# Kernel optimization log

Hardware: AMD Instinct MI355X
Metric: run time of the kernel (lower is better)

## Reference

```python
import jax, jax.numpy as jnp
import numpy as np

N_NODES = 50000
N_EDGES = 800000
NFEAT, NHID, NOUT = 512, 256, 64


def setup_inputs() -> dict:
    key = jax.random.key(0)
    ks = jax.random.split(key, 8)
    x = jax.random.normal(ks[0], (N_NODES, NFEAT), dtype=jnp.float32)
    w1 = jax.random.normal(ks[1], (NFEAT, NHID), dtype=jnp.float32) * (1.0 / np.sqrt(NFEAT))
    b1 = jnp.zeros((NHID,), dtype=jnp.float32)
    w2 = jax.random.normal(ks[2], (NHID, NOUT), dtype=jnp.float32) * (1.0 / np.sqrt(NHID))
    b2 = jnp.zeros((NOUT,), dtype=jnp.float32)
    edge_w = jax.random.uniform(ks[3], (N_EDGES,), dtype=jnp.float32)
    row = jnp.sort(jax.random.randint(ks[4], (N_EDGES,), 0, N_NODES, dtype=jnp.int32))
    col = jax.random.randint(ks[5], (N_EDGES,), 0, N_NODES, dtype=jnp.int32)
    return {"x": x, "w1": w1, "b1": b1, "w2": w2, "b2": b2,
            "edge_w": edge_w, "row": row, "col": col}


def _spmm(edge_w, row, col, h, n_nodes):
    # sparse adj (COO) @ dense h : gather source rows, scale, scatter-add to dest
    msgs = h[col] * edge_w[:, None]          # [E, d]
    return jax.ops.segment_sum(msgs, row, num_segments=n_nodes)


def reference(x, w1, b1, w2, b2, edge_w, row, col):
    n = x.shape[0]
    # layer 1: support = x @ W1; out = adj @ support + b1; relu
    h = jnp.matmul(x, w1)                    # [N, nhid]
    h = _spmm(edge_w, row, col, h, n) + b1
    h = jax.nn.relu(h)
    # layer 2
    h = jnp.matmul(h, w2)                    # [N, nout]
    out = _spmm(edge_w, row, col, h, n) + b2
    return out
```

## Files before the change

kernel.cpp:

```cpp
#include <hip/hip_runtime.h>

#define N_NODES 50000
#define MP      50048
#define N_EDGES 800000
#define NFEAT   512
#define NHID    256
#define NOUT    64

typedef __bf16 bf16x8 __attribute__((ext_vector_type(8)));
typedef float  f32x4  __attribute__((ext_vector_type(4)));

#define GLOAD_LDS16(g, l) __builtin_amdgcn_global_load_lds(                    \
    (const __attribute__((address_space(1))) void*)(g),                        \
    (__attribute__((address_space(3))) void*)(l), 16, 0, 0)

__device__ __forceinline__ unsigned short f2bf(float f) {
    __bf16 b = (__bf16)f;
    return __builtin_bit_cast(unsigned short, b);
}

__global__ void build_rowptr(const int* __restrict__ row, int* __restrict__ rp) {
    int r = blockIdx.x * blockDim.x + threadIdx.x;
    if (r > N_NODES) return;
    int lo = 0, hi = N_EDGES;
    while (lo < hi) {
        int mid = (lo + hi) >> 1;
        if (row[mid] < r) lo = mid + 1; else hi = mid;
    }
    rp[r] = lo;
}

__global__ __launch_bounds__(256) void conv_x(const float* __restrict__ x,
                                              __bf16* __restrict__ xb) {
    size_t i = ((size_t)blockIdx.x * 256 + threadIdx.x) * 8;
    unsigned short u[8];
    if (i < (size_t)N_NODES * NFEAT) {
        float4 a = *(const float4*)(x + i);
        float4 b = *(const float4*)(x + i + 4);
        u[0] = f2bf(a.x); u[1] = f2bf(a.y); u[2] = f2bf(a.z); u[3] = f2bf(a.w);
        u[4] = f2bf(b.x); u[5] = f2bf(b.y); u[6] = f2bf(b.z); u[7] = f2bf(b.w);
    } else {
        #pragma unroll
        for (int j = 0; j < 8; j++) u[j] = 0;
    }
    uint4 o;
    o.x = (unsigned)u[0] | ((unsigned)u[1] << 16);
    o.y = (unsigned)u[2] | ((unsigned)u[3] << 16);
    o.z = (unsigned)u[4] | ((unsigned)u[5] << 16);
    o.w = (unsigned)u[6] | ((unsigned)u[7] << 16);
    *(uint4*)(xb + i) = o;
}

__global__ void conv_w1t(const float* __restrict__ w1, __bf16* __restrict__ w1t) {
    int o = blockIdx.x * blockDim.x + threadIdx.x;
    int n = o >> 9, k = o & 511;
    w1t[o] = (__bf16)w1[(size_t)k * NHID + n];
}

__global__ void conv_w2t(const float* __restrict__ w2, __bf16* __restrict__ w2t) {
    int o = blockIdx.x * blockDim.x + threadIdx.x;
    int n = o >> 8, k = o & 255;
    w2t[o] = (__bf16)w2[(size_t)k * NOUT + n];
}

__global__ void zero_h1pad(__bf16* __restrict__ h1) {
    int i = blockIdx.x * blockDim.x + threadIdx.x;
    h1[(size_t)N_NODES * NHID + i] = (__bf16)0.f;
}

__global__ __launch_bounds__(256) void gemm1_mfma(const __bf16* __restrict__ A,
                                                  const __bf16* __restrict__ Bt,
                                                  __bf16* __restrict__ C) {
    __shared__ __bf16 As[128 * 32];
    __shared__ __bf16 Bs[128 * 32];
    const int t = threadIdx.x;
    const int w = t >> 6, l = t & 63;
    const int wm = w >> 1, wn = w & 1;
    const int ml = l & 15, quad = l >> 4;
    const int row0 = blockIdx.x * 128;
    const int col0 = blockIdx.y * 128;

    f32x4 acc[4][4] = {};

    for (int k0 = 0; k0 < NFEAT; k0 += 32) {
        #pragma unroll
        for (int i = 0; i < 2; i++) {
            int q = (w * 2 + i) * 64 + l;
            int r = q >> 2, cc = (q & 3) * 8;
            GLOAD_LDS16(A  + (size_t)(row0 + r) * NFEAT + k0 + cc, As + (w * 2 + i) * 512);
            GLOAD_LDS16(Bt + (size_t)(col0 + r) * NFEAT + k0 + cc, Bs + (w * 2 + i) * 512);
        }
        __syncthreads();
        bf16x8 af[4], bfr[4];
        #pragma unroll
        for (int mi = 0; mi < 4; mi++)
            af[mi] = *(const bf16x8*)(As + (wm * 64 + mi * 16 + ml) * 32 + quad * 8);
        #pragma unroll
        for (int ni = 0; ni < 4; ni++)
            bfr[ni] = *(const bf16x8*)(Bs + (wn * 64 + ni * 16 + ml) * 32 + quad * 8);
        #pragma unroll
        for (int mi = 0; mi < 4; mi++)
            #pragma unroll
            for (int ni = 0; ni < 4; ni++)
                acc[mi][ni] = __builtin_amdgcn_mfma_f32_16x16x32_bf16(
                    af[mi], bfr[ni], acc[mi][ni], 0, 0, 0);
        __syncthreads();
    }

    #pragma unroll
    for (int mi = 0; mi < 4; mi++) {
        int gr = row0 + wm * 64 + mi * 16 + quad * 4;
        #pragma unroll
        for (int ni = 0; ni < 4; ni++) {
            int gc = col0 + wn * 64 + ni * 16 + ml;
            #pragma unroll
            for (int r2 = 0; r2 < 4; r2++)
                C[(size_t)(gr + r2) * NHID + gc] = (__bf16)acc[mi][ni][r2];
        }
    }
}

__global__ __launch_bounds__(256) void gemm2_mfma(const __bf16* __restrict__ A,
                                                  const __bf16* __restrict__ Bt,
                                                  float* __restrict__ C) {
    __shared__ __bf16 As[128 * 32];
    __shared__ __bf16 Bs[64 * 32];
    const int t = threadIdx.x;
    const int w = t >> 6, l = t & 63;
    const int ml = l & 15, quad = l >> 4;
    const int row0 = blockIdx.x * 128;

    f32x4 acc[2][4] = {};

    for (int k0 = 0; k0 < NHID; k0 += 32) {
        #pragma unroll
        for (int i = 0; i < 2; i++) {
            int q = (w * 2 + i) * 64 + l;
            int r = q >> 2, cc = (q & 3) * 8;
            GLOAD_LDS16(A + (size_t)(row0 + r) * NHID + k0 + cc, As + (w * 2 + i) * 512);
        }
        {
            int q = w * 64 + l;
            int r = q >> 2, cc = (q & 3) * 8;
            GLOAD_LDS16(Bt + (size_t)r * NHID + k0 + cc, Bs + w * 512);
        }
        __syncthreads();
        bf16x8 af[2], bfr[4];
        #pragma unroll
        for (int mi = 0; mi < 2; mi++)
            af[mi] = *(const bf16x8*)(As + (w * 32 + mi * 16 + ml) * 32 + quad * 8);
        #pragma unroll
        for (int ni = 0; ni < 4; ni++)
            bfr[ni] = *(const bf16x8*)(Bs + (ni * 16 + ml) * 32 + quad * 8);
        #pragma unroll
        for (int mi = 0; mi < 2; mi++)
            #pragma unroll
            for (int ni = 0; ni < 4; ni++)
                acc[mi][ni] = __builtin_amdgcn_mfma_f32_16x16x32_bf16(
                    af[mi], bfr[ni], acc[mi][ni], 0, 0, 0);
        __syncthreads();
    }

    #pragma unroll
    for (int mi = 0; mi < 2; mi++) {
        int gr = row0 + w * 32 + mi * 16 + quad * 4;
        #pragma unroll
        for (int ni = 0; ni < 4; ni++) {
            int gc = ni * 16 + ml;
            #pragma unroll
            for (int r2 = 0; r2 < 4; r2++)
                C[(size_t)(gr + r2) * NOUT + gc] = acc[mi][ni][r2];
        }
    }
}

__global__ __launch_bounds__(256) void spmm1_wave(const __bf16* __restrict__ h0,
                                                  const float* __restrict__ ew,
                                                  const int* __restrict__ col,
                                                  const int* __restrict__ rp,
                                                  const float* __restrict__ b1,
                                                  __bf16* __restrict__ h1) {
    const int n    = blockIdx.x * 4 + (threadIdx.x >> 6);
    const int lane = threadIdx.x & 63;
    const int half = lane >> 5;
    const int fl   = lane & 31;
    const int s = rp[n], e = rp[n + 1];

    float acc[8] = {};
    int i = s + half;
    for (; i + 2 < e; i += 4) {
        int   c0 = col[i],   c1 = col[i + 2];
        float w0 = ew[i],    w1 = ew[i + 2];
        uint4 v0 = *(const uint4*)(h0 + (size_t)c0 * NHID + fl * 8);
        uint4 v1 = *(const uint4*)(h0 + (size_t)c1 * NHID + fl * 8);
        const unsigned* p0 = &v0.x;
        const unsigned* p1 = &v1.x;
        #pragma unroll
        for (int j = 0; j < 4; j++) {
            acc[2*j+0] += w0 * __builtin_bit_cast(float, p0[j] << 16);
            acc[2*j+1] += w0 * __builtin_bit_cast(float, p0[j] & 0xffff0000u);
            acc[2*j+0] += w1 * __builtin_bit_cast(float, p1[j] << 16);
            acc[2*j+1] += w1 * __builtin_bit_cast(float, p1[j] & 0xffff0000u);
        }
    }
    for (; i < e; i += 2) {
        int   c0 = col[i];
        float w0 = ew[i];
        uint4 v0 = *(const uint4*)(h0 + (size_t)c0 * NHID + fl * 8);
        const unsigned* p0 = &v0.x;
        #pragma unroll
        for (int j = 0; j < 4; j++) {
            acc[2*j+0] += w0 * __builtin_bit_cast(float, p0[j] << 16);
            acc[2*j+1] += w0 * __builtin_bit_cast(float, p0[j] & 0xffff0000u);
        }
    }

    #pragma unroll
    for (int j = 0; j < 8; j++)
        acc[j] += __shfl_down(acc[j], 32, 64);

    if (half == 0) {
        unsigned short u[8];
        #pragma unroll
        for (int j = 0; j < 8; j++) {
            float v = acc[j] + b1[fl * 8 + j];
            u[j] = f2bf(v > 0.f ? v : 0.f);
        }
        uint4 o;
        o.x = (unsigned)u[0] | ((unsigned)u[1] << 16);
        o.y = (unsigned)u[2] | ((unsigned)u[3] << 16);
        o.z = (unsigned)u[4] | ((unsigned)u[5] << 16);
        o.w = (unsigned)u[6] | ((unsigned)u[7] << 16);
        *(uint4*)(h1 + (size_t)n * NHID + fl * 8) = o;
    }
}

__global__ __launch_bounds__(256) void spmm2_wave(const float* __restrict__ h2,
                                                  const float* __restrict__ ew,
                                                  const int* __restrict__ col,
                                                  const int* __restrict__ rp,
                                                  const float* __restrict__ b2,
                                                  float* __restrict__ out) {
    const int n    = blockIdx.x * 4 + (threadIdx.x >> 6);
    const int lane = threadIdx.x & 63;
    const int s = rp[n], e = rp[n + 1];
    float acc = 0.f;
    int i = s;
    for (; i + 3 < e; i += 4) {
        int   c0 = col[i],  c1 = col[i+1], c2 = col[i+2], c3 = col[i+3];
        float w0 = ew[i],   w1 = ew[i+1],  w2 = ew[i+2],  w3 = ew[i+3];
        float v0 = h2[(size_t)c0 * NOUT + lane];
        float v1 = h2[(size_t)c1 * NOUT + lane];
        float v2 = h2[(size_t)c2 * NOUT + lane];
        float v3 = h2[(size_t)c3 * NOUT + lane];
        acc += w0 * v0 + w1 * v1 + w2 * v2 + w3 * v3;
    }
    for (; i < e; i++) {
        acc += ew[i] * h2[(size_t)col[i] * NOUT + lane];
    }
    out[(size_t)n * NOUT + lane] = acc + b2[lane];
}

extern "C" void kernel_launch(void* const* d_in, const int* in_sizes, int n_in,
                              void* d_out, int out_size, void* d_ws, size_t ws_size,
                              hipStream_t stream) {
    const float* x   = (const float*)d_in[0];
    const float* w1  = (const float*)d_in[1];
    const float* b1  = (const float*)d_in[2];
    const float* w2  = (const float*)d_in[3];
    const float* b2  = (const float*)d_in[4];
    const float* ew  = (const float*)d_in[5];
    const int*   row = (const int*)d_in[6];
    const int*   col = (const int*)d_in[7];
    float* out = (float*)d_out;

    char* ws = (char*)d_ws;
    size_t off = 256 * 1024;
    int*    rp  = (int*)ws;
    __bf16* xb  = (__bf16*)(ws + off);               off += (size_t)MP * NFEAT * 2;
    __bf16* h0  = (__bf16*)(ws + off);               off += (size_t)MP * NHID * 2;
    __bf16* w1t = (__bf16*)(ws + off);               off += (size_t)NHID * NFEAT * 2;
    __bf16* w2t = (__bf16*)(ws + off);
    __bf16* h1  = xb;
    float*  h2  = (float*)h0;

    build_rowptr<<<(N_NODES + 1 + 255) / 256, 256, 0, stream>>>(row, rp);
    conv_x  <<<(size_t)MP * NFEAT / 2048, 256, 0, stream>>>(x, xb);
    conv_w1t<<<NHID * NFEAT / 256, 256, 0, stream>>>(w1, w1t);
    conv_w2t<<<NOUT * NHID / 256, 256, 0, stream>>>(w2, w2t);

    gemm1_mfma<<<dim3(MP / 128, NHID / 128), 256, 0, stream>>>(xb, w1t, h0);

    zero_h1pad<<<(MP - N_NODES) * NHID / 256, 256, 0, stream>>>(h1);
    spmm1_wave<<<N_NODES / 4, 256, 0, stream>>>(h0, ew, col, rp, b1, h1);

    gemm2_mfma<<<MP / 128, 256, 0, stream>>>(h1, w2t, h2);

    spmm2_wave<<<N_NODES / 4, 256, 0, stream>>>(h2, ew, col, rp, b2, out);
}
```

Measured before the change: 316.2 us.

## Fuse x conversion into GEMM1, merge prep kernels, use bf16 h2 in SpMM2

Merges rowptr construction, weight transposes and pad zeroing into one prep kernel. GEMM1 now reads fp32 x directly and converts it to bf16 while staging into LDS, covering the full 256-column N in one block, so the separate conversion pass and the second read of x for the other column half go away. GEMM2 writes h2 in bf16, which halves SpMM2 gather traffic, and SpMM2 gives each 16-lane group its own edges with a shuffle reduction at the end. SpMM1 unrolls to four gathers per iteration. The trade-offs are lower precision in h2, synchronous non-async A loads and a larger per-thread accumulator set in GEMM1 (128 floats), which may hurt occupancy.

```diff
diff --git a/kernel.cpp b/kernel.cpp
--- a/kernel.cpp
+++ b/kernel.cpp
@@ -19,89 +19,93 @@
     return __builtin_bit_cast(unsigned short, b);
 }
 
-__global__ void build_rowptr(const int* __restrict__ row, int* __restrict__ rp) {
-    int r = blockIdx.x * blockDim.x + threadIdx.x;
-    if (r > N_NODES) return;
-    int lo = 0, hi = N_EDGES;
-    while (lo < hi) {
-        int mid = (lo + hi) >> 1;
-        if (row[mid] < r) lo = mid + 1; else hi = mid;
-    }
-    rp[r] = lo;
-}
-
-__global__ __launch_bounds__(256) void conv_x(const float* __restrict__ x,
-                                              __bf16* __restrict__ xb) {
-    size_t i = ((size_t)blockIdx.x * 256 + threadIdx.x) * 8;
-    unsigned short u[8];
-    if (i < (size_t)N_NODES * NFEAT) {
-        float4 a = *(const float4*)(x + i);
-        float4 b = *(const float4*)(x + i + 4);
-        u[0] = f2bf(a.x); u[1] = f2bf(a.y); u[2] = f2bf(a.z); u[3] = f2bf(a.w);
-        u[4] = f2bf(b.x); u[5] = f2bf(b.y); u[6] = f2bf(b.z); u[7] = f2bf(b.w);
+__global__ __launch_bounds__(256) void prep(const int* __restrict__ row,
+                                            int* __restrict__ rp,
+                                            const float* __restrict__ w1,
+                                            __bf16* __restrict__ w1t,
+                                            const float* __restrict__ w2,
+                                            __bf16* __restrict__ w2t,
+                                            __bf16* __restrict__ h1) {
+    const int b = blockIdx.x, t = threadIdx.x;
+    if (b < 196) {
+        int r = b * 256 + t;
+        if (r <= N_NODES) {
+            int lo = 0, hi = N_EDGES;
+            while (lo < hi) {
+                int mid = (lo + hi) >> 1;
+                if (row[mid] < r) lo = mid + 1; else hi = mid;
+            }
+            rp[r] = lo;
+        }
+    } else if (b < 708) {
+        int o = (b - 196) * 256 + t;
+        w1t[o] = (__bf16)w1[(size_t)(o & 511) * NHID + (o >> 9)];
+    } else if (b < 772) {
+        int o = (b - 708) * 256 + t;
+        w2t[o] = (__bf16)w2[(size_t)(o & 255) * NOUT + (o >> 8)];
     } else {
-        #pragma unroll
-        for (int j = 0; j < 8; j++) u[j] = 0;
-    }
-    uint4 o;
-    o.x = (unsigned)u[0] | ((unsigned)u[1] << 16);
-    o.y = (unsigned)u[2] | ((unsigned)u[3] << 16);
-    o.z = (unsigned)u[4] | ((unsigned)u[5] << 16);
-    o.w = (unsigned)u[6] | ((unsigned)u[7] << 16);
-    *(uint4*)(xb + i) = o;
-}
-
-__global__ void conv_w1t(const float* __restrict__ w1, __bf16* __restrict__ w1t) {
-    int o = blockIdx.x * blockDim.x + threadIdx.x;
-    int n = o >> 9, k = o & 511;
-    w1t[o] = (__bf16)w1[(size_t)k * NHID + n];
-}
-
-__global__ void conv_w2t(const float* __restrict__ w2, __bf16* __restrict__ w2t) {
-    int o = blockIdx.x * blockDim.x + threadIdx.x;
-    int n = o >> 8, k = o & 255;
-    w2t[o] = (__bf16)w2[(size_t)k * NOUT + n];
-}
-
-__global__ void zero_h1pad(__bf16* __restrict__ h1) {
-    int i = blockIdx.x * blockDim.x + threadIdx.x;
-    h1[(size_t)N_NODES * NHID + i] = (__bf16)0.f;
-}
-
-__global__ __launch_bounds__(256) void gemm1_mfma(const __bf16* __restrict__ A,
-                                                  const __bf16* __restrict__ Bt,
-                                                  __bf16* __restrict__ C) {
+        int o = (b - 772) * 256 + t;
+        h1[(size_t)N_NODES * NHID + o] = (__bf16)0.f;
+    }
+}
+
+__global__ __launch_bounds__(256) void gemm1_fused(const float* __restrict__ X,
+                                                   const __bf16* __restrict__ Bt,
+                                                   __bf16* __restrict__ C) {
     __shared__ __bf16 As[128 * 32];
-    __shared__ __bf16 Bs[128 * 32];
+    __shared__ __bf16 Bs[256 * 32];
     const int t = threadIdx.x;
     const int w = t >> 6, l = t & 63;
     const int wm = w >> 1, wn = w & 1;
     const int ml = l & 15, quad = l >> 4;
     const int row0 = blockIdx.x * 128;
-    const int col0 = blockIdx.y * 128;
-
-    f32x4 acc[4][4] = {};
+
+    f32x4 acc[4][8] = {};
 
     for (int k0 = 0; k0 < NFEAT; k0 += 32) {
         #pragma unroll
-        for (int i = 0; i < 2; i++) {
-            int q = (w * 2 + i) * 64 + l;
+        for (int it = 0; it < 4; it++) {
+            int q = it * 256 + w * 64 + l;
             int r = q >> 2, cc = (q & 3) * 8;
-            GLOAD_LDS16(A  + (size_t)(row0 + r) * NFEAT + k0 + cc, As + (w * 2 + i) * 512);
-            GLOAD_LDS16(Bt + (size_t)(col0 + r) * NFEAT + k0 + cc, Bs + (w * 2 + i) * 512);
+            GLOAD_LDS16(Bt + (size_t)r * NFEAT + k0 + cc,
+                        Bs + (size_t)(it * 256 + w * 64) * 8);
+        }
+        #pragma unroll
+        for (int it = 0; it < 2; it++) {
+            int q = it * 256 + t;
+            int r = q >> 2, cc = (q & 3) * 8;
+            int gr = row0 + r;
+            unsigned short u[8];
+            if (gr < N_NODES) {
+                const float* src = X + (size_t)gr * NFEAT + k0 + cc;
+                float4 a = *(const float4*)src;
+                float4 b = *(const float4*)(src + 4);
+                u[0] = f2bf(a.x); u[1] = f2bf(a.y); u[2] = f2bf(a.z); u[3] = f2bf(a.w);
+                u[4] = f2bf(b.x); u[5] = f2bf(b.y); u[6] = f2bf(b.z); u[7] = f2bf(b.w);
+            } else {
+                #pragma unroll
+                for (int j = 0; j < 8; j++) u[j] = 0;
+            }
+            uint4 o;
+            o.x = (unsigned)u[0] | ((unsigned)u[1] << 16);
+            o.y = (unsigned)u[2] | ((unsigned)u[3] << 16);
+            o.z = (unsigned)u[4] | ((unsigned)u[5] << 16);
+            o.w = (unsigned)u[6] | ((unsigned)u[7] << 16);
+            *(uint4*)(As + (size_t)q * 8) = o;
         }
         __syncthreads();
-        bf16x8 af[4], bfr[4];
+
+        bf16x8 af[4], bfr[8];
         #pragma unroll
         for (int mi = 0; mi < 4; mi++)
             af[mi] = *(const bf16x8*)(As + (wm * 64 + mi * 16 + ml) * 32 + quad * 8);
         #pragma unroll
-        for (int ni = 0; ni < 4; ni++)
-            bfr[ni] = *(const bf16x8*)(Bs + (wn * 64 + ni * 16 + ml) * 32 + quad * 8);
+        for (int ni = 0; ni < 8; ni++)
+            bfr[ni] = *(const bf16x8*)(Bs + (wn * 128 + ni * 16 + ml) * 32 + quad * 8);
         #pragma unroll
         for (int mi = 0; mi < 4; mi++)
             #pragma unroll
-            for (int ni = 0; ni < 4; ni++)
+            for (int ni = 0; ni < 8; ni++)
                 acc[mi][ni] = __builtin_amdgcn_mfma_f32_16x16x32_bf16(
                     af[mi], bfr[ni], acc[mi][ni], 0, 0, 0);
         __syncthreads();
@@ -111,8 +115,8 @@
     for (int mi = 0; mi < 4; mi++) {
         int gr = row0 + wm * 64 + mi * 16 + quad * 4;
         #pragma unroll
-        for (int ni = 0; ni < 4; ni++) {
-            int gc = col0 + wn * 64 + ni * 16 + ml;
+        for (int ni = 0; ni < 8; ni++) {
+            int gc = wn * 128 + ni * 16 + ml;
             #pragma unroll
             for (int r2 = 0; r2 < 4; r2++)
                 C[(size_t)(gr + r2) * NHID + gc] = (__bf16)acc[mi][ni][r2];
@@ -122,7 +126,7 @@
 
 __global__ __launch_bounds__(256) void gemm2_mfma(const __bf16* __restrict__ A,
                                                   const __bf16* __restrict__ Bt,
-                                                  float* __restrict__ C) {
+                                                  __bf16* __restrict__ C) {
     __shared__ __bf16 As[128 * 32];
     __shared__ __bf16 Bs[64 * 32];
     const int t = threadIdx.x;
@@ -169,7 +173,7 @@
             int gc = ni * 16 + ml;
             #pragma unroll
             for (int r2 = 0; r2 < 4; r2++)
-                C[(size_t)(gr + r2) * NOUT + gc] = acc[mi][ni][r2];
+                C[(size_t)(gr + r2) * NOUT + gc] = (__bf16)acc[mi][ni][r2];
         }
     }
 }
@@ -188,19 +192,25 @@
 
     float acc[8] = {};
     int i = s + half;
-    for (; i + 2 < e; i += 4) {
-        int   c0 = col[i],   c1 = col[i + 2];
-        float w0 = ew[i],    w1 = ew[i + 2];
+    for (; i + 6 < e; i += 8) {
+        int   c0 = col[i],     c1 = col[i + 2], c2 = col[i + 4], c3 = col[i + 6];
+        float w0 = ew[i],      w1 = ew[i + 2],  w2 = ew[i + 4],  w3 = ew[i + 6];
         uint4 v0 = *(const uint4*)(h0 + (size_t)c0 * NHID + fl * 8);
         uint4 v1 = *(const uint4*)(h0 + (size_t)c1 * NHID + fl * 8);
-        const unsigned* p0 = &v0.x;
-        const unsigned* p1 = &v1.x;
+        uint4 v2 = *(const uint4*)(h0 + (size_t)c2 * NHID + fl * 8);
+        uint4 v3 = *(const uint4*)(h0 + (size_t)c3 * NHID + fl * 8);
+        const unsigned* p0 = &v0.x; const unsigned* p1 = &v1.x;
+        const unsigned* p2 = &v2.x; const unsigned* p3 = &v3.x;
         #pragma unroll
         for (int j = 0; j < 4; j++) {
-            acc[2*j+0] += w0 * __builtin_bit_cast(float, p0[j] << 16);
-            acc[2*j+1] += w0 * __builtin_bit_cast(float, p0[j] & 0xffff0000u);
-            acc[2*j+0] += w1 * __builtin_bit_cast(float, p1[j] << 16);
-            acc[2*j+1] += w1 * __builtin_bit_cast(float, p1[j] & 0xffff0000u);
+            acc[2*j+0] += w0 * __builtin_bit_cast(float, p0[j] << 16)
+                        + w1 * __builtin_bit_cast(float, p1[j] << 16)
+                        + w2 * __builtin_bit_cast(float, p2[j] << 16)
+                        + w3 * __builtin_bit_cast(float, p3[j] << 16);
+            acc[2*j+1] += w0 * __builtin_bit_cast(float, p0[j] & 0xffff0000u)
+                        + w1 * __builtin_bit_cast(float, p1[j] & 0xffff0000u)
+                        + w2 * __builtin_bit_cast(float, p2[j] & 0xffff0000u)
+                        + w3 * __builtin_bit_cast(float, p3[j] & 0xffff0000u);
         }
     }
     for (; i < e; i += 2) {
@@ -235,7 +245,7 @@
     }
 }
 
-__global__ __launch_bounds__(256) void spmm2_wave(const float* __restrict__ h2,
+__global__ __launch_bounds__(256) void spmm2_wave(const __bf16* __restrict__ h2,
                                                   const float* __restrict__ ew,
                                                   const int* __restrict__ col,
                                                   const int* __restrict__ rp,
@@ -243,22 +253,45 @@
                                                   float* __restrict__ out) {
     const int n    = blockIdx.x * 4 + (threadIdx.x >> 6);
     const int lane = threadIdx.x & 63;
+    const int g    = lane >> 4;
+    const int fl   = lane & 15;
     const int s = rp[n], e = rp[n + 1];
-    float acc = 0.f;
-    int i = s;
-    for (; i + 3 < e; i += 4) {
-        int   c0 = col[i],  c1 = col[i+1], c2 = col[i+2], c3 = col[i+3];
-        float w0 = ew[i],   w1 = ew[i+1],  w2 = ew[i+2],  w3 = ew[i+3];
-        float v0 = h2[(size_t)c0 * NOUT + lane];
-        float v1 = h2[(size_t)c1 * NOUT + lane];
-        float v2 = h2[(size_t)c2 * NOUT + lane];
-        float v3 = h2[(size_t)c3 * NOUT + lane];
-        acc += w0 * v0 + w1 * v1 + w2 * v2 + w3 * v3;
-    }
-    for (; i < e; i++) {
-        acc += ew[i] * h2[(size_t)col[i] * NOUT + lane];
-    }
-    out[(size_t)n * NOUT + lane] = acc + b2[lane];
+
+    float a0 = 0.f, a1 = 0.f, a2 = 0.f, a3 = 0.f;
+    int i = s + g;
+    for (; i + 4 < e; i += 8) {
+        int   c0 = col[i];     float w0 = ew[i];
+        int   c1 = col[i + 4]; float w1 = ew[i + 4];
+        uint2 v0 = *(const uint2*)(h2 + (size_t)c0 * NOUT + fl * 4);
+        uint2 v1 = *(const uint2*)(h2 + (size_t)c1 * NOUT + fl * 4);
+        a0 += w0 * __builtin_bit_cast(float, v0.x << 16)
+            + w1 * __builtin_bit_cast(float, v1.x << 16);
+        a1 += w0 * __builtin_bit_cast(float, v0.x & 0xffff0000u)
+            + w1 * __builtin_bit_cast(float, v1.x & 0xffff0000u);
+        a2 += w0 * __builtin_bit_cast(float, v0.y << 16)
+            + w1 * __builtin_bit_cast(float, v1.y << 16);
+        a3 += w0 * __builtin_bit_cast(float, v0.y & 0xffff0000u)
+            + w1 * __builtin_bit_cast(float, v1.y & 0xffff0000u);
+    }
+    for (; i < e; i += 4) {
+        int   c0 = col[i]; float w0 = ew[i];
+        uint2 v0 = *(const uint2*)(h2 + (size_t)c0 * NOUT + fl * 4);
+        a0 += w0 * __builtin_bit_cast(float, v0.x << 16);
+        a1 += w0 * __builtin_bit_cast(float, v0.x & 0xffff0000u);
+        a2 += w0 * __builtin_bit_cast(float, v0.y << 16);
+        a3 += w0 * __builtin_bit_cast(float, v0.y & 0xffff0000u);
+    }
+
+    a0 += __shfl_down(a0, 32, 64); a1 += __shfl_down(a1, 32, 64);
+    a2 += __shfl_down(a2, 32, 64); a3 += __shfl_down(a3, 32, 64);
+    a0 += __shfl_down(a0, 16, 64); a1 += __shfl_down(a1, 16, 64);
+    a2 += __shfl_down(a2, 16, 64); a3 += __shfl_down(a3, 16, 64);
+
+    if (lane < 16) {
+        float4 bb = *(const float4*)(b2 + fl * 4);
+        float4 o = make_float4(a0 + bb.x, a1 + bb.y, a2 + bb.z, a3 + bb.w);
+        *(float4*)(out + (size_t)n * NOUT + fl * 4) = o;
+    }
 }
 
 extern "C" void kernel_launch(void* const* d_in, const int* in_sizes, int n_in,
@@ -275,23 +308,18 @@
     float* out = (float*)d_out;
 
     char* ws = (char*)d_ws;
-    size_t off = 256 * 1024;
-    int*    rp  = (int*)ws;
-    __bf16* xb  = (__bf16*)(ws + off);               off += (size_t)MP * NFEAT * 2;
-    __bf16* h0  = (__bf16*)(ws + off);               off += (size_t)MP * NHID * 2;
-    __bf16* w1t = (__bf16*)(ws + off);               off += (size_t)NHID * NFEAT * 2;
-    __bf16* w2t = (__bf16*)(ws + off);
-    __bf16* h1  = xb;
-    float*  h2  = (float*)h0;
-
-    build_rowptr<<<(N_NODES + 1 + 255) / 256, 256, 0, stream>>>(row, rp);
-    conv_x  <<<(size_t)MP * NFEAT / 2048, 256, 0, stream>>>(x, xb);
-    conv_w1t<<<NHID * NFEAT / 256, 256, 0, stream>>>(w1, w1t);
-    conv_w2t<<<NOUT * NHID / 256, 256, 0, stream>>>(w2, w2t);
-
-    gemm1_mfma<<<dim3(MP / 128, NHID / 128), 256, 0, stream>>>(xb, w1t, h0);
-
-    zero_h1pad<<<(MP - N_NODES) * NHID / 256, 256, 0, stream>>>(h1);
+    size_t off = 0;
+    int*    rp  = (int*)(ws + off);   off += 256 * 1024;
+    __bf16* w1t = (__bf16*)(ws + off); off += (size_t)NHID * NFEAT * 2;
+    __bf16* w2t = (__bf16*)(ws + off); off += (size_t)NOUT * NHID * 2;
+    __bf16* h0  = (__bf16*)(ws + off); off += (size_t)MP * NHID * 2;
+    __bf16* h1  = (__bf16*)(ws + off); off += (size_t)MP * NHID * 2;
+    __bf16* h2  = (__bf16*)(ws + off);
+
+    prep<<<820, 256, 0, stream>>>(row, rp, w1, w1t, w2, w2t, h1);
+
+    gemm1_fused<<<MP / 128, 256, 0, stream>>>(x, w1t, h0);
+
     spmm1_wave<<<N_NODES / 4, 256, 0, stream>>>(h0, ew, col, rp, b1, h1);
 
     gemm2_mfma<<<MP / 128, 256, 0, stream>>>(h1, w2t, h2);
```

New measurement: 298.3 us. 1.06x faster.
